# Kernel optimization log

Hardware: AMD Instinct MI355X
Metric: run time of the kernel (lower is better)

Reference implementation:

```python
import jax, jax.numpy as jnp
import numpy as np


def setup_inputs() -> dict:
    key = jax.random.key(0)
    ks = jax.random.split(key, 6)
    B, U, T, E, H = 8, 128, 256, 128, 128
    # Xavier-uniform scale for linear layers
    def xavier(k, shape):
        fan_in, fan_out = shape[0], shape[1]
        lim = jnp.sqrt(6.0 / (fan_in + fan_out))
        return jax.random.uniform(k, shape, jnp.float32, -lim, lim)
    return {
        "ue": jax.random.normal(ks[0], (B, U, E), jnp.float32),
        "te": jax.random.normal(ks[1], (B, T, E), jnp.float32),
        "ge": jax.random.normal(ks[2], (B, E), jnp.float32),
        "W1": xavier(ks[3], (3 * E, H)),
        "b1": jnp.zeros((H,), jnp.float32),
        "W2": xavier(ks[4], (H, H)),
        "b2": jnp.zeros((H,), jnp.float32),
        "W3": xavier(ks[5], (H, 1)),
        "b3": jnp.zeros((1,), jnp.float32),
    }


def reference(ue, te, ge, W1, b1, W2, b2, W3, b3):
    # Equivalent to cat([u,t,g], -1) @ W1: decompose W1 into per-source blocks
    # and broadcast-add, avoiding the [B,U,T,3E] intermediate.
    E = ue.shape[-1]
    W1u, W1t, W1g = W1[:E], W1[E:2 * E], W1[2 * E:]
    h = (jnp.einsum("bue,eh->buh", ue, W1u)[:, :, None, :]
         + jnp.einsum("bte,eh->bth", te, W1t)[:, None, :, :]
         + (ge @ W1g)[:, None, None, :]
         + b1)                                   # [B,U,T,H]
    h = jax.nn.gelu(h, approximate=False)        # torch nn.GELU default = exact erf
    h = jax.nn.gelu(h @ W2 + b2, approximate=False)
    logits = (h @ W3 + b3)[..., 0]               # [B,U,T]
    B, U, T = logits.shape
    return logits.reshape(B, U * T)
```

## Files before the change

### kernel.cpp

```cpp
#include <hip/hip_runtime.h>
#include <hip/hip_bf16.h>
#include <math.h>

#define E_ 128
#define H_ 128
#define B_ 8
#define U_ 128
#define T_ 256
#define LDK 136

typedef short short8 __attribute__((ext_vector_type(8)));
typedef unsigned short ushort8_t __attribute__((ext_vector_type(8)));
typedef float floatx4 __attribute__((ext_vector_type(4)));

__device__ __forceinline__ unsigned short f2bf(float f) {
    union { __hip_bfloat16 b; unsigned short u; } cv;
    cv.b = __float2bfloat16(f);
    return cv.u;
}

__device__ __forceinline__ float gelu_fast(float x) {
    float x2 = x * x;
    float p = x * __builtin_fmaf(x2, 0.1029407583f, 2.3022586210f);
    float e = __builtin_amdgcn_exp2f(-p);
    return x * __builtin_amdgcn_rcpf(1.0f + e);
}

__global__ __launch_bounds__(256) void stage1_kernel(
    const float* __restrict__ ue, const float* __restrict__ te,
    const float* __restrict__ ge, const float* __restrict__ W1,
    const float* __restrict__ b1, const float* __restrict__ W2,
    float* __restrict__ hu_ws, float* __restrict__ ht_ws,
    float* __restrict__ gu_ws, unsigned short* __restrict__ w2t_ws)
{
    const int blk = blockIdx.x;
    const int tid = threadIdx.x;

    if (blk < 24) {
        __shared__ unsigned short a_s[128][LDK];
        __shared__ unsigned short w_s[128][LDK];
        const float* __restrict__ A;
        const float* __restrict__ W;
        float* __restrict__ outp;
        if (blk < 8) { A = ue + (size_t)blk * 128 * E_;        W = W1;            outp = hu_ws + (size_t)blk * 128 * H_; }
        else         { A = te + (size_t)(blk - 8) * 128 * E_;  W = W1 + E_ * H_;  outp = ht_ws + (size_t)(blk - 8) * 128 * H_; }

        const float4* __restrict__ Av = (const float4*)A;
        #pragma unroll
        for (int i = 0; i < 16; i++) {
            const int v = tid + i * 256;
            const int row = v >> 5, c = (v & 31) * 4;
            const float4 f = Av[v];
            ushort4 u4 = make_ushort4(f2bf(f.x), f2bf(f.y), f2bf(f.z), f2bf(f.w));
            *(ushort4*)(&a_s[row][c]) = u4;
        }
        const float4* __restrict__ Wv = (const float4*)W;
        #pragma unroll
        for (int i = 0; i < 16; i++) {
            const int v = tid + i * 256;
            const int k = v >> 5, n = (v & 31) * 4;
            const float4 f = Wv[v];
            w_s[n + 0][k] = f2bf(f.x);
            w_s[n + 1][k] = f2bf(f.y);
            w_s[n + 2][k] = f2bf(f.z);
            w_s[n + 3][k] = f2bf(f.w);
        }
        __syncthreads();

        const int wave = tid >> 6, lane = tid & 63;
        const int quad = lane >> 4, l16 = lane & 15;
        const int r0 = wave * 32 + l16;

        floatx4 acc[2][8];
        #pragma unroll
        for (int m = 0; m < 2; m++)
            #pragma unroll
            for (int nt = 0; nt < 8; nt++) acc[m][nt] = (floatx4){0.f, 0.f, 0.f, 0.f};

        #pragma unroll
        for (int kk = 0; kk < 4; kk++) {
            const int k0 = kk * 32 + quad * 8;
            short8 af0 = *(const short8*)(&a_s[r0][k0]);
            short8 af1 = *(const short8*)(&a_s[r0 + 16][k0]);
            #pragma unroll
            for (int nt = 0; nt < 8; nt++) {
                short8 bf = *(const short8*)(&w_s[nt * 16 + l16][k0]);
                acc[0][nt] = __builtin_amdgcn_mfma_f32_16x16x32_bf16(af0, bf, acc[0][nt], 0, 0, 0);
                acc[1][nt] = __builtin_amdgcn_mfma_f32_16x16x32_bf16(af1, bf, acc[1][nt], 0, 0, 0);
            }
        }
        #pragma unroll
        for (int m = 0; m < 2; m++) {
            const int rowb = wave * 32 + m * 16 + quad * 4;
            #pragma unroll
            for (int nt = 0; nt < 8; nt++) {
                const int col = nt * 16 + l16;
                #pragma unroll
                for (int r = 0; r < 4; r++)
                    outp[(size_t)(rowb + r) * H_ + col] = acc[m][nt][r];
            }
        }
    } else if (blk < 28) {
        __shared__ float ge_s[2][E_];
        const int rbase = (blk - 24) * 2;
        const int half = tid >> 7, n = tid & 127;
        ge_s[half][n] = ge[(rbase + half) * E_ + n];
        __syncthreads();
        const float* __restrict__ W1g = W1 + 2 * E_ * H_;
        float acc = b1[n];
        #pragma unroll 8
        for (int e = 0; e < E_; e++)
            acc = __builtin_fmaf(ge_s[half][e], W1g[e * H_ + n], acc);
        gu_ws[(rbase + half) * H_ + n] = acc;
    } else {
        const int base = (blk - 28) * 2048;
        #pragma unroll
        for (int i = 0; i < 8; i++) {
            const int o = base + tid + i * 256;
            const int n = o >> 7, k = o & 127;
            w2t_ws[o] = f2bf(W2[k * H_ + n]);
        }
    }
}

__global__ __launch_bounds__(256, 4) void stage2_kernel(
    const float* __restrict__ hu_ws, const float* __restrict__ ht_ws,
    const float* __restrict__ gu_ws,
    const unsigned short* __restrict__ w2t_ws,
    const float* __restrict__ b2, const float* __restrict__ W3,
    const float* __restrict__ b3, float* __restrict__ out)
{
    __shared__ unsigned short w2s[H_][LDK];
    __shared__ float hu_s[H_];
    __shared__ float b2_s[H_];
    __shared__ float w3_s[H_];

    const int tid = threadIdx.x;
    const int t0 = blockIdx.x * 128;
    const int u  = blockIdx.y;
    const int b  = blockIdx.z;

    for (int g = tid; g < (H_ * H_) / 8; g += 256) {
        const int n = g >> 4;
        const int c = (g & 15) * 8;
        *(ushort8_t*)(&w2s[n][c]) = *(const ushort8_t*)(w2t_ws + n * H_ + c);
    }
    if (tid < H_) {
        hu_s[tid] = hu_ws[((b << 7) + u) * H_ + tid] + gu_ws[b * H_ + tid];
        b2_s[tid] = b2[tid];
        w3_s[tid] = W3[tid];
    }
    __syncthreads();

    const int wave = tid >> 6, lane = tid & 63;
    const int quad = lane >> 4, l16 = lane & 15;

    const int rowA = t0 + wave * 32 + l16;
    const float* __restrict__ htrow0 = ht_ws + ((size_t)(b * T_) + rowA) * H_;
    const float* __restrict__ htrow1 = htrow0 + 16 * H_;

    floatx4 acc[2][8];
    #pragma unroll
    for (int m = 0; m < 2; m++)
        #pragma unroll
        for (int nt = 0; nt < 8; nt++) acc[m][nt] = (floatx4){0.f, 0.f, 0.f, 0.f};

    #pragma unroll
    for (int kk = 0; kk < 4; kk++) {
        const int k0 = kk * 32 + quad * 8;
        const float4 h0 = *(const float4*)(&hu_s[k0]);
        const float4 h1 = *(const float4*)(&hu_s[k0 + 4]);
        const float4 a00 = *(const float4*)(htrow0 + k0);
        const float4 a01 = *(const float4*)(htrow0 + k0 + 4);
        const float4 a10 = *(const float4*)(htrow1 + k0);
        const float4 a11 = *(const float4*)(htrow1 + k0 + 4);
        short8 af0, af1;
        af0[0] = (short)f2bf(gelu_fast(a00.x + h0.x));
        af0[1] = (short)f2bf(gelu_fast(a00.y + h0.y));
        af0[2] = (short)f2bf(gelu_fast(a00.z + h0.z));
        af0[3] = (short)f2bf(gelu_fast(a00.w + h0.w));
        af0[4] = (short)f2bf(gelu_fast(a01.x + h1.x));
        af0[5] = (short)f2bf(gelu_fast(a01.y + h1.y));
        af0[6] = (short)f2bf(gelu_fast(a01.z + h1.z));
        af0[7] = (short)f2bf(gelu_fast(a01.w + h1.w));
        af1[0] = (short)f2bf(gelu_fast(a10.x + h0.x));
        af1[1] = (short)f2bf(gelu_fast(a10.y + h0.y));
        af1[2] = (short)f2bf(gelu_fast(a10.z + h0.z));
        af1[3] = (short)f2bf(gelu_fast(a10.w + h0.w));
        af1[4] = (short)f2bf(gelu_fast(a11.x + h1.x));
        af1[5] = (short)f2bf(gelu_fast(a11.y + h1.y));
        af1[6] = (short)f2bf(gelu_fast(a11.z + h1.z));
        af1[7] = (short)f2bf(gelu_fast(a11.w + h1.w));
        #pragma unroll
        for (int nt = 0; nt < 8; nt++) {
            short8 bf = *(const short8*)(&w2s[nt * 16 + l16][k0]);
            acc[0][nt] = __builtin_amdgcn_mfma_f32_16x16x32_bf16(af0, bf, acc[0][nt], 0, 0, 0);
            acc[1][nt] = __builtin_amdgcn_mfma_f32_16x16x32_bf16(af1, bf, acc[1][nt], 0, 0, 0);
        }
    }

    const float b3v = b3[0];
    float psum[2][4] = {{0.f, 0.f, 0.f, 0.f}, {0.f, 0.f, 0.f, 0.f}};
    #pragma unroll
    for (int nt = 0; nt < 8; nt++) {
        const int n = nt * 16 + l16;
        const float bb = b2_s[n];
        const float ww = w3_s[n];
        #pragma unroll
        for (int m = 0; m < 2; m++)
            #pragma unroll
            for (int r = 0; r < 4; r++)
                psum[m][r] += gelu_fast(acc[m][nt][r] + bb) * ww;
    }
    #pragma unroll
    for (int s = 8; s >= 1; s >>= 1) {
        #pragma unroll
        for (int m = 0; m < 2; m++)
            #pragma unroll
            for (int r = 0; r < 4; r++)
                psum[m][r] += __shfl_xor(psum[m][r], s, 64);
    }
    if (l16 == 0) {
        #pragma unroll
        for (int m = 0; m < 2; m++) {
            const int rowb = t0 + wave * 32 + m * 16 + quad * 4;
            float4 o = make_float4(psum[m][0] + b3v, psum[m][1] + b3v,
                                   psum[m][2] + b3v, psum[m][3] + b3v);
            *(float4*)(out + (size_t)((b << 7) + u) * T_ + rowb) = o;
        }
    }
}

extern "C" void kernel_launch(void* const* d_in, const int* in_sizes, int n_in,
                              void* d_out, int out_size, void* d_ws, size_t ws_size,
                              hipStream_t stream)
{
    const float* ue = (const float*)d_in[0];
    const float* te = (const float*)d_in[1];
    const float* ge = (const float*)d_in[2];
    const float* W1 = (const float*)d_in[3];
    const float* b1 = (const float*)d_in[4];
    const float* W2 = (const float*)d_in[5];
    const float* b2 = (const float*)d_in[6];
    const float* W3 = (const float*)d_in[7];
    const float* b3 = (const float*)d_in[8];
    float* out = (float*)d_out;

    char* ws = (char*)d_ws;
    float* hu_ws = (float*)ws;
    float* ht_ws = (float*)(ws + 512 * 1024);
    unsigned short* w2t_ws = (unsigned short*)(ws + 1536 * 1024);
    float* gu_ws = (float*)(ws + 1568 * 1024);

    stage1_kernel<<<dim3(36), dim3(256), 0, stream>>>(
        ue, te, ge, W1, b1, W2, hu_ws, ht_ws, gu_ws, w2t_ws);
    stage2_kernel<<<dim3(T_ / 128, U_, B_), dim3(256), 0, stream>>>(
        hu_ws, ht_ws, gu_ws, w2t_ws, b2, W3, b3, out);
}
```

Before: 102.9 us.

## Store ht in bf16, stage it through swizzled LDS, drop padding

The ht projection is now written in bf16 instead of fp32, which halves the bytes stage2 reads for it. Stage2 loads the 128-row ht tile into LDS with coalesced 16-byte loads, replacing the per-lane strided global reads. Padded LDS arrays are replaced by an XOR swizzle to avoid bank conflicts. In exchange, LDS use per block doubles (launch bounds lowered from 4 to 2 blocks), which reduces occupancy, and ht gains an extra bf16 rounding before the add.

```diff
diff --git a/kernel.cpp b/kernel.cpp
--- a/kernel.cpp
+++ b/kernel.cpp
@@ -7,16 +7,24 @@
 #define B_ 8
 #define U_ 128
 #define T_ 256
-#define LDK 136
 
 typedef short short8 __attribute__((ext_vector_type(8)));
-typedef unsigned short ushort8_t __attribute__((ext_vector_type(8)));
+typedef unsigned short ushortx8 __attribute__((ext_vector_type(8)));
 typedef float floatx4 __attribute__((ext_vector_type(4)));
 
 __device__ __forceinline__ unsigned short f2bf(float f) {
     union { __hip_bfloat16 b; unsigned short u; } cv;
     cv.b = __float2bfloat16(f);
     return cv.u;
+}
+__device__ __forceinline__ float bf2f(unsigned short u) {
+    union { unsigned int u; float f; } cv;
+    cv.u = ((unsigned int)u) << 16;
+    return cv.f;
+}
+
+__device__ __forceinline__ int sw(int row, int cblk) {
+    return row * 128 + (((cblk ^ (row & 15)) << 3));
 }
 
 __device__ __forceinline__ float gelu_fast(float x) {
@@ -30,40 +38,41 @@
     const float* __restrict__ ue, const float* __restrict__ te,
     const float* __restrict__ ge, const float* __restrict__ W1,
     const float* __restrict__ b1, const float* __restrict__ W2,
-    float* __restrict__ hu_ws, float* __restrict__ ht_ws,
+    float* __restrict__ hu_ws, unsigned short* __restrict__ ht_bf,
     float* __restrict__ gu_ws, unsigned short* __restrict__ w2t_ws)
 {
     const int blk = blockIdx.x;
     const int tid = threadIdx.x;
 
     if (blk < 24) {
-        __shared__ unsigned short a_s[128][LDK];
-        __shared__ unsigned short w_s[128][LDK];
+        __shared__ unsigned short a_s[128 * 128];
+        __shared__ unsigned short w_s[128 * 128];
         const float* __restrict__ A;
         const float* __restrict__ W;
-        float* __restrict__ outp;
-        if (blk < 8) { A = ue + (size_t)blk * 128 * E_;        W = W1;            outp = hu_ws + (size_t)blk * 128 * H_; }
-        else         { A = te + (size_t)(blk - 8) * 128 * E_;  W = W1 + E_ * H_;  outp = ht_ws + (size_t)(blk - 8) * 128 * H_; }
+        const bool is_ue = (blk < 8);
+        if (is_ue) { A = ue + (size_t)blk * 128 * E_;       W = W1; }
+        else       { A = te + (size_t)(blk - 8) * 128 * E_; W = W1 + E_ * H_; }
 
         const float4* __restrict__ Av = (const float4*)A;
         #pragma unroll
         for (int i = 0; i < 16; i++) {
             const int v = tid + i * 256;
-            const int row = v >> 5, c = (v & 31) * 4;
+            const int row = v >> 5, c4 = (v & 31) * 4;
             const float4 f = Av[v];
             ushort4 u4 = make_ushort4(f2bf(f.x), f2bf(f.y), f2bf(f.z), f2bf(f.w));
-            *(ushort4*)(&a_s[row][c]) = u4;
+            *(ushort4*)(&a_s[sw(row, c4 >> 3) + (c4 & 7)]) = u4;
         }
         const float4* __restrict__ Wv = (const float4*)W;
         #pragma unroll
         for (int i = 0; i < 16; i++) {
             const int v = tid + i * 256;
-            const int k = v >> 5, n = (v & 31) * 4;
+            const int k = v >> 5, n4 = (v & 31) * 4;
             const float4 f = Wv[v];
-            w_s[n + 0][k] = f2bf(f.x);
-            w_s[n + 1][k] = f2bf(f.y);
-            w_s[n + 2][k] = f2bf(f.z);
-            w_s[n + 3][k] = f2bf(f.w);
+            const int c = k >> 3, off = k & 7;
+            w_s[sw(n4 + 0, c) + off] = f2bf(f.x);
+            w_s[sw(n4 + 1, c) + off] = f2bf(f.y);
+            w_s[sw(n4 + 2, c) + off] = f2bf(f.z);
+            w_s[sw(n4 + 3, c) + off] = f2bf(f.w);
         }
         __syncthreads();
 
@@ -79,25 +88,41 @@
 
         #pragma unroll
         for (int kk = 0; kk < 4; kk++) {
-            const int k0 = kk * 32 + quad * 8;
-            short8 af0 = *(const short8*)(&a_s[r0][k0]);
-            short8 af1 = *(const short8*)(&a_s[r0 + 16][k0]);
+            const int c = kk * 4 + quad;
+            short8 af0 = *(const short8*)(&a_s[sw(r0, c)]);
+            short8 af1 = *(const short8*)(&a_s[sw(r0 + 16, c)]);
             #pragma unroll
             for (int nt = 0; nt < 8; nt++) {
-                short8 bf = *(const short8*)(&w_s[nt * 16 + l16][k0]);
+                short8 bf = *(const short8*)(&w_s[sw(nt * 16 + l16, c)]);
                 acc[0][nt] = __builtin_amdgcn_mfma_f32_16x16x32_bf16(af0, bf, acc[0][nt], 0, 0, 0);
                 acc[1][nt] = __builtin_amdgcn_mfma_f32_16x16x32_bf16(af1, bf, acc[1][nt], 0, 0, 0);
             }
         }
-        #pragma unroll
-        for (int m = 0; m < 2; m++) {
-            const int rowb = wave * 32 + m * 16 + quad * 4;
-            #pragma unroll
-            for (int nt = 0; nt < 8; nt++) {
-                const int col = nt * 16 + l16;
+        if (is_ue) {
+            float* __restrict__ outp = hu_ws + (size_t)blk * 128 * H_;
+            #pragma unroll
+            for (int m = 0; m < 2; m++) {
+                const int rowb = wave * 32 + m * 16 + quad * 4;
                 #pragma unroll
-                for (int r = 0; r < 4; r++)
-                    outp[(size_t)(rowb + r) * H_ + col] = acc[m][nt][r];
+                for (int nt = 0; nt < 8; nt++) {
+                    const int col = nt * 16 + l16;
+                    #pragma unroll
+                    for (int r = 0; r < 4; r++)
+                        outp[(size_t)(rowb + r) * H_ + col] = acc[m][nt][r];
+                }
+            }
+        } else {
+            unsigned short* __restrict__ outp = ht_bf + (size_t)(blk - 8) * 128 * H_;
+            #pragma unroll
+            for (int m = 0; m < 2; m++) {
+                const int rowb = wave * 32 + m * 16 + quad * 4;
+                #pragma unroll
+                for (int nt = 0; nt < 8; nt++) {
+                    const int col = nt * 16 + l16;
+                    #pragma unroll
+                    for (int r = 0; r < 4; r++)
+                        outp[(size_t)(rowb + r) * H_ + col] = f2bf(acc[m][nt][r]);
+                }
             }
         }
     } else if (blk < 28) {
@@ -123,14 +148,15 @@
     }
 }
 
-__global__ __launch_bounds__(256, 4) void stage2_kernel(
-    const float* __restrict__ hu_ws, const float* __restrict__ ht_ws,
+__global__ __launch_bounds__(256, 2) void stage2_kernel(
+    const float* __restrict__ hu_ws, const unsigned short* __restrict__ ht_bf,
     const float* __restrict__ gu_ws,
     const unsigned short* __restrict__ w2t_ws,
     const float* __restrict__ b2, const float* __restrict__ W3,
     const float* __restrict__ b3, float* __restrict__ out)
 {
-    __shared__ unsigned short w2s[H_][LDK];
+    __shared__ unsigned short w2s[128 * 128];
+    __shared__ unsigned short ht_s[128 * 128];
     __shared__ float hu_s[H_];
     __shared__ float b2_s[H_];
     __shared__ float w3_s[H_];
@@ -140,10 +166,18 @@
     const int u  = blockIdx.y;
     const int b  = blockIdx.z;
 
-    for (int g = tid; g < (H_ * H_) / 8; g += 256) {
-        const int n = g >> 4;
-        const int c = (g & 15) * 8;
-        *(ushort8_t*)(&w2s[n][c]) = *(const ushort8_t*)(w2t_ws + n * H_ + c);
+    #pragma unroll
+    for (int i = 0; i < 8; i++) {
+        const int v = tid + i * 256;
+        const int n = v >> 4, c = v & 15;
+        *(ushortx8*)(&w2s[sw(n, c)]) = *(const ushortx8*)(w2t_ws + n * 128 + c * 8);
+    }
+    const unsigned short* __restrict__ htg = ht_bf + ((size_t)(b * T_ + t0)) * H_;
+    #pragma unroll
+    for (int i = 0; i < 8; i++) {
+        const int v = tid + i * 256;
+        const int row = v >> 4, c = v & 15;
+        *(ushortx8*)(&ht_s[sw(row, c)]) = *(const ushortx8*)(htg + row * 128 + c * 8);
     }
     if (tid < H_) {
         hu_s[tid] = hu_ws[((b << 7) + u) * H_ + tid] + gu_ws[b * H_ + tid];
@@ -154,10 +188,7 @@
 
     const int wave = tid >> 6, lane = tid & 63;
     const int quad = lane >> 4, l16 = lane & 15;
-
-    const int rowA = t0 + wave * 32 + l16;
-    const float* __restrict__ htrow0 = ht_ws + ((size_t)(b * T_) + rowA) * H_;
-    const float* __restrict__ htrow1 = htrow0 + 16 * H_;
+    const int r0 = wave * 32 + l16;
 
     floatx4 acc[2][8];
     #pragma unroll
@@ -167,33 +198,22 @@
 
     #pragma unroll
     for (int kk = 0; kk < 4; kk++) {
-        const int k0 = kk * 32 + quad * 8;
+        const int c = kk * 4 + quad;
+        const int k0 = c << 3;
+        ushortx8 u0 = *(const ushortx8*)(&ht_s[sw(r0, c)]);
+        ushortx8 u1 = *(const ushortx8*)(&ht_s[sw(r0 + 16, c)]);
         const float4 h0 = *(const float4*)(&hu_s[k0]);
         const float4 h1 = *(const float4*)(&hu_s[k0 + 4]);
-        const float4 a00 = *(const float4*)(htrow0 + k0);
-        const float4 a01 = *(const float4*)(htrow0 + k0 + 4);
-        const float4 a10 = *(const float4*)(htrow1 + k0);
-        const float4 a11 = *(const float4*)(htrow1 + k0 + 4);
+        const float hv[8] = {h0.x, h0.y, h0.z, h0.w, h1.x, h1.y, h1.z, h1.w};
         short8 af0, af1;
-        af0[0] = (short)f2bf(gelu_fast(a00.x + h0.x));
-        af0[1] = (short)f2bf(gelu_fast(a00.y + h0.y));
-        af0[2] = (short)f2bf(gelu_fast(a00.z + h0.z));
-        af0[3] = (short)f2bf(gelu_fast(a00.w + h0.w));
-        af0[4] = (short)f2bf(gelu_fast(a01.x + h1.x));
-        af0[5] = (short)f2bf(gelu_fast(a01.y + h1.y));
-        af0[6] = (short)f2bf(gelu_fast(a01.z + h1.z));
-        af0[7] = (short)f2bf(gelu_fast(a01.w + h1.w));
-        af1[0] = (short)f2bf(gelu_fast(a10.x + h0.x));
-        af1[1] = (short)f2bf(gelu_fast(a10.y + h0.y));
-        af1[2] = (short)f2bf(gelu_fast(a10.z + h0.z));
-        af1[3] = (short)f2bf(gelu_fast(a10.w + h0.w));
-        af1[4] = (short)f2bf(gelu_fast(a11.x + h1.x));
-        af1[5] = (short)f2bf(gelu_fast(a11.y + h1.y));
-        af1[6] = (short)f2bf(gelu_fast(a11.z + h1.z));
-        af1[7] = (short)f2bf(gelu_fast(a11.w + h1.w));
+        #pragma unroll
+        for (int j = 0; j < 8; j++) {
+            af0[j] = (short)f2bf(gelu_fast(bf2f(u0[j]) + hv[j]));
+            af1[j] = (short)f2bf(gelu_fast(bf2f(u1[j]) + hv[j]));
+        }
         #pragma unroll
         for (int nt = 0; nt < 8; nt++) {
-            short8 bf = *(const short8*)(&w2s[nt * 16 + l16][k0]);
+            short8 bf = *(const short8*)(&w2s[sw(nt * 16 + l16, c)]);
             acc[0][nt] = __builtin_amdgcn_mfma_f32_16x16x32_bf16(af0, bf, acc[0][nt], 0, 0, 0);
             acc[1][nt] = __builtin_amdgcn_mfma_f32_16x16x32_bf16(af1, bf, acc[1][nt], 0, 0, 0);
         }
@@ -248,12 +268,12 @@
 
     char* ws = (char*)d_ws;
     float* hu_ws = (float*)ws;
-    float* ht_ws = (float*)(ws + 512 * 1024);
-    unsigned short* w2t_ws = (unsigned short*)(ws + 1536 * 1024);
-    float* gu_ws = (float*)(ws + 1568 * 1024);
+    unsigned short* ht_bf = (unsigned short*)(ws + 512 * 1024);
+    unsigned short* w2t_ws = (unsigned short*)(ws + 1024 * 1024);
+    float* gu_ws = (float*)(ws + 1056 * 1024);
 
     stage1_kernel<<<dim3(36), dim3(256), 0, stream>>>(
-        ue, te, ge, W1, b1, W2, hu_ws, ht_ws, gu_ws, w2t_ws);
+        ue, te, ge, W1, b1, W2, hu_ws, ht_bf, gu_ws, w2t_ws);
     stage2_kernel<<<dim3(T_ / 128, U_, B_), dim3(256), 0, stream>>>(
-        hu_ws, ht_ws, gu_ws, w2t_ws, b2, W3, b3, out);
-}
+        hu_ws, ht_bf, gu_ws, w2t_ws, b2, W3, b3, out);
+}
```

Result: slower. 105.2 us (+2.2%).
